# Kernel tuning notes

Measured on AMD Instinct MI355X. Metric: run time of the kernel, lower is better.

The kernel has to match this reference:

```python
import jax, jax.numpy as jnp
import numpy as np

ID_LENGTH = 4   # number of identity images cached in the id bank
HEADS = 20      # SDXL attention heads at channel 1280
SA32 = 0.5


def setup_inputs() -> dict:
    key = jax.random.key(0)
    ks = jax.random.split(key, 7)
    B2, T, C = 8, 576, 1280            # 2*id_length images, 576 tokens each (768/32)^2
    S = ID_LENGTH * T                   # 2304 grouped sequence length
    hidden_states = jax.random.normal(ks[0], (B2, T, C), jnp.float32)
    # cal_attn_mask_xl: one random row pattern repeated, with each image's own
    # block forced True (sliced to the [:id_length*T, :id_length*T] write-mode mask)
    row_pat = jax.random.uniform(ks[1], (1, S)) < SA32
    mask = jnp.tile(row_pat, (S, 1))
    img = jnp.arange(S) // T
    mask = mask | (img[:, None] == img[None, :])
    w = lambda k: jax.random.normal(k, (C, C), jnp.float32) * 0.02
    return {
        "hidden_states": hidden_states,
        "mask": mask,
        "Wq": w(ks[2]), "Wk": w(ks[3]), "Wv": w(ks[4]), "Wo": w(ks[5]),
        "bo": jnp.zeros((C,), jnp.float32),
    }


def reference(hidden_states, mask, Wq, Wk, Wv, Wo, bo):
    # __call1__ path: regroup [2*id_length, T, C] -> [2, id_length*T, C]
    B2, T, C = hidden_states.shape
    hs = hidden_states.reshape(2, ID_LENGTH * T, C)
    hd = C // HEADS

    def split_heads(x):  # [2, S, C] -> [2, H, S, hd]
        return x.reshape(2, -1, HEADS, hd).transpose(0, 2, 1, 3)

    q = split_heads(hs @ Wq)
    k = split_heads(hs @ Wk)   # write mode: encoder_hidden_states == hidden_states
    v = split_heads(hs @ Wv)

    scores = jnp.einsum('bhqd,bhkd->bhqk', q, k) / jnp.sqrt(jnp.asarray(hd, q.dtype))
    scores = jnp.where(mask[None, None], scores, jnp.finfo(scores.dtype).min)
    attnw = jax.nn.softmax(scores, axis=-1)
    out = jnp.einsum('bhqk,bhkd->bhqd', attnw, v)
    out = out.transpose(0, 2, 1, 3).reshape(2, -1, C)
    out = out @ Wo + bo                 # attn.to_out[0]
    return out.reshape(B2, T, C)
```

## Files before the change

kernel.cpp:

```cpp
#include <hip/hip_runtime.h>
#include <hip/hip_bf16.h>
#include <stdint.h>
#include <math.h>

#define S_TOT 2304
#define C_DIM 1280
#define NHEAD 20
#define HD    64
#define M_TOT 4608
#define BH_STRIDE (S_TOT * HD)
#define SC_ROWS 2624
#define KC_STRIDE (SC_ROWS * 64)
#define LOG2E 1.44269504088896f
#define C_SC  (0.125f * LOG2E)
#define MFIX  12.0f

typedef __attribute__((ext_vector_type(8))) short bf16x8;
typedef __attribute__((ext_vector_type(4))) float f32x4;

__device__ __forceinline__ short f2bf(float f) {
    union { float f; uint32_t u; } v; v.f = f;
    uint32_t r = v.u + 0x7FFFu + ((v.u >> 16) & 1u);
    return (short)(r >> 16);
}

__device__ __forceinline__ uint32_t pack2bf(float a, float b) {
    __hip_bfloat162 h = __float22bfloat162_rn(make_float2(a, b));
    union { __hip_bfloat162 h; uint32_t u; } cv; cv.h = h; return cv.u;
}

__device__ __forceinline__ f32x4 zero4() {
    f32x4 z; z[0] = 0.f; z[1] = 0.f; z[2] = 0.f; z[3] = 0.f; return z;
}

__device__ __forceinline__ void gload_lds16(const void* g, void* l) {
    __builtin_amdgcn_global_load_lds(
        (const __attribute__((address_space(1))) uint32_t*)g,
        (__attribute__((address_space(3))) uint32_t*)l, 16, 0, 0);
}

__global__ __launch_bounds__(256)
void prologue(const float* __restrict__ hs, short* __restrict__ hsb,
              const float* __restrict__ W0, const float* __restrict__ W1,
              const float* __restrict__ W2, const float* __restrict__ W3,
              short* __restrict__ T0, short* __restrict__ T1,
              short* __restrict__ T2, short* __restrict__ T3,
              const int* __restrict__ mask, int* __restrict__ hdr,
              int* __restrict__ destmap) {
    __shared__ float tile[32][33];
    __shared__ unsigned long long wbits[36];
    __shared__ int pp[36], dd[36], hb[9];

    const int bx = blockIdx.x;
    const int t = threadIdx.x;

    if (bx < 2880) {
        const int i = bx * 256 + t;
        const float4 v0 = reinterpret_cast<const float4*>(hs)[i * 2];
        const float4 v1 = reinterpret_cast<const float4*>(hs)[i * 2 + 1];
        bf16x8 o;
        o[0] = f2bf(v0.x); o[1] = f2bf(v0.y); o[2] = f2bf(v0.z); o[3] = f2bf(v0.w);
        o[4] = f2bf(v1.x); o[5] = f2bf(v1.y); o[6] = f2bf(v1.z); o[7] = f2bf(v1.w);
        reinterpret_cast<bf16x8*>(hsb)[i] = o;
    } else if (bx < 9280) {
        int id = bx - 2880;
        const int z = id / 1600; id -= z * 1600;
        const int by = id / 40, bxx = id - by * 40;
        const float* W; short* T;
        switch (z) {
            case 0:  W = W0; T = T0; break;
            case 1:  W = W1; T = T1; break;
            case 2:  W = W2; T = T2; break;
            default: W = W3; T = T3; break;
        }
        const int tx = t & 31, ty = t >> 5;
        const int k0 = by * 32, n0 = bxx * 32;
#pragma unroll
        for (int i = 0; i < 4; ++i)
            tile[ty + i * 8][tx] = W[(size_t)(k0 + ty + i * 8) * C_DIM + n0 + tx];
        __syncthreads();
#pragma unroll
        for (int i = 0; i < 4; ++i)
            T[(size_t)(n0 + ty + i * 8) * C_DIM + k0 + tx] = f2bf(tile[tx][ty + i * 8]);
    } else {
        for (int it = 0; it < 9; ++it) {
            const int k = it * 256 + t;
            const int src = (k < 1152) ? 1152 : 0;
            const bool pat = mask[(size_t)src * S_TOT + k] != 0;
            unsigned long long b = __ballot(pat);
            if ((t & 63) == 0) wbits[it * 4 + (t >> 6)] = b;
        }
        __syncthreads();
        if (t == 0) {
            int pcum = 0, dcum[4] = {0, 0, 0, 0};
            for (int wdx = 0; wdx < 36; ++wdx) {
                const int img = wdx / 9;
                const int pc = __popcll(wbits[wdx]);
                pp[wdx] = pcum; dd[wdx] = dcum[img];
                pcum += pc; dcum[img] += 64 - pc;
            }
            hb[0] = pcum;
            int base = (pcum + 63) & ~63;
            for (int i = 0; i < 4; ++i) {
                hb[1 + i] = base; hb[5 + i] = dcum[i];
                base += (dcum[i] + 63) & ~63;
            }
            for (int i = 0; i < 9; ++i) hdr[i] = hb[i];
        }
        __syncthreads();
        if (t < 36) {
            const unsigned long long w64 = wbits[t];
            const int img = t / 9;
            const int pbase = pp[t], dbase = hb[1 + img] + dd[t];
            int pc = 0, dc = 0;
            for (int b = 0; b < 64; ++b) {
                if ((w64 >> b) & 1) destmap[t * 64 + b] = pbase + (pc++);
                else                destmap[t * 64 + b] = dbase + (dc++);
            }
        }
    }
}

__global__ __launch_bounds__(256)
void zero_pads(const int* __restrict__ hdr, short* __restrict__ Kc,
               short* __restrict__ Vr) {
    const int bh = blockIdx.x;
    const int t = threadIdx.x;
    short* Kb = Kc + (size_t)bh * KC_STRIDE;
    short* Vb = Vr + (size_t)bh * KC_STRIDE;
    for (int seg = 0; seg < 5; ++seg) {
        const int cnt = (seg == 0) ? hdr[0] : hdr[4 + seg];
        const int sb  = (seg == 0) ? 0      : hdr[seg];
        const int s0 = sb + cnt;
        const int nrows = ((cnt + 63) & ~63) - cnt;
        for (int idx = t; idx < nrows * 64; idx += 256) {
            const int r = idx >> 6, d = idx & 63;
            Kb[(size_t)(s0 + r) * 64 + d] = 0;
            Vb[(size_t)(s0 + r) * 64 + d] = 0;
        }
    }
}

__global__ __launch_bounds__(256)
void transp_v(const short* __restrict__ Vr, short* __restrict__ Vc) {
    __shared__ short tile[64][72];
    const int bh = blockIdx.y;
    const int s0 = blockIdx.x * 64;
    const int t = threadIdx.x;
    const short* src = Vr + (size_t)bh * KC_STRIDE;
    short* dst = Vc + (size_t)bh * KC_STRIDE;

#pragma unroll
    for (int i = 0; i < 2; ++i) {
        const int e = (i * 256 + t) * 8;
        const int r = e >> 6, c = e & 63;
        bf16x8 v = *(const bf16x8*)(src + (size_t)(s0 + r) * 64 + c);
        *(bf16x8*)&tile[r][c] = v;
    }
    __syncthreads();
    const int d = t & 63, c0 = (t >> 6) * 16;
    short tmp[16];
#pragma unroll
    for (int j = 0; j < 16; ++j) tmp[j] = tile[c0 + j][d];
    *(bf16x8*)(dst + (size_t)d * SC_ROWS + s0 + c0) = *(const bf16x8*)tmp;
    *(bf16x8*)(dst + (size_t)d * SC_ROWS + s0 + c0 + 8) = *(const bf16x8*)(tmp + 8);
}

__device__ __forceinline__ void gemm_core(const short* __restrict__ A,
                                          const short* __restrict__ Wt,
                                          int m0, int n0,
                                          f32x4 acc[4][4],
                                          short* AsB, short* BsB) {
    const int t = threadIdx.x;
    const int lane = t & 63, w = t >> 6;
    const int g = lane >> 4, l15 = lane & 15;
    const int wm = w >> 1, wn = w & 1;

#pragma unroll
    for (int mi = 0; mi < 4; ++mi)
#pragma unroll
        for (int ni = 0; ni < 4; ++ni) acc[mi][ni] = zero4();

    auto stage = [&](int k0, int buf) {
#pragma unroll
        for (int i = 0; i < 4; ++i) {
            const int F = i * 4096 + t * 16;
            const int row = F >> 7;
            const int b = F & 127;
            const int colb = b ^ ((row & 7) << 4);
            gload_lds16((const char*)A + ((size_t)(m0 + row) * C_DIM + k0) * 2 + colb,
                        (char*)AsB + buf * 16384 + F);
            gload_lds16((const char*)Wt + ((size_t)(n0 + row) * C_DIM + k0) * 2 + colb,
                        (char*)BsB + buf * 16384 + F);
        }
    };

    stage(0, 0);
    asm volatile("s_waitcnt vmcnt(0)" ::: "memory");
    __builtin_amdgcn_s_barrier();
    __builtin_amdgcn_sched_barrier(0);

    int cur = 0;
    for (int k0 = 0; k0 < C_DIM; k0 += 64) {
        if (k0 + 64 < C_DIM) stage(k0 + 64, cur ^ 1);
        const char* Ac = (const char*)AsB + cur * 16384;
        const char* Bc = (const char*)BsB + cur * 16384;
#pragma unroll
        for (int ks = 0; ks < 2; ++ks) {
            const int kb = ks * 64 + g * 16;
            bf16x8 af[4], bfr[4];
#pragma unroll
            for (int mi = 0; mi < 4; ++mi) {
                const int row = wm * 64 + mi * 16 + l15;
                af[mi] = *(const bf16x8*)(Ac + row * 128 + (kb ^ ((row & 7) << 4)));
            }
#pragma unroll
            for (int ni = 0; ni < 4; ++ni) {
                const int row = wn * 64 + ni * 16 + l15;
                bfr[ni] = *(const bf16x8*)(Bc + row * 128 + (kb ^ ((row & 7) << 4)));
            }
            __builtin_amdgcn_s_setprio(1);
#pragma unroll
            for (int mi = 0; mi < 4; ++mi)
#pragma unroll
                for (int ni = 0; ni < 4; ++ni)
                    acc[mi][ni] = __builtin_amdgcn_mfma_f32_16x16x32_bf16(
                        af[mi], bfr[ni], acc[mi][ni], 0, 0, 0);
            __builtin_amdgcn_s_setprio(0);
        }
        asm volatile("s_waitcnt vmcnt(0)" ::: "memory");
        __builtin_amdgcn_s_barrier();
        __builtin_amdgcn_sched_barrier(0);
        cur ^= 1;
    }
}

__global__ __launch_bounds__(256)
void gemm_qkv(const short* __restrict__ hsb,
              const short* __restrict__ Wtq, const short* __restrict__ Wtk,
              const short* __restrict__ Wtv, const int* __restrict__ destmap,
              short* __restrict__ Qb, short* __restrict__ Kc, short* __restrict__ Vr) {
    __shared__ short As[2 * 128 * 64];
    __shared__ short Bs[2 * 128 * 64];
    __shared__ int dm[128];
    const int z = blockIdx.z;
    const short* Wt = (z == 0) ? Wtq : (z == 1) ? Wtk : Wtv;
    const int n0 = blockIdx.x * 128, m0 = blockIdx.y * 128;
    const int t = threadIdx.x;

    if (z != 0 && t < 128) {
        const int s0 = (m0 >= S_TOT) ? m0 - S_TOT : m0;
        dm[t] = destmap[s0 + t];
    }

    f32x4 acc[4][4];
    gemm_core(hsb, Wt, m0, n0, acc, As, Bs);

    const int lane = t & 63, w = t >> 6, g = lane >> 4, l15 = lane & 15;
    const int wm = w >> 1, wn = w & 1;
#pragma unroll
    for (int mi = 0; mi < 4; ++mi)
#pragma unroll
        for (int ni = 0; ni < 4; ++ni)
#pragma unroll
            for (int r = 0; r < 4; ++r) {
                const int m = m0 + wm * 64 + mi * 16 + g * 4 + r;
                const int n = n0 + wn * 64 + ni * 16 + l15;
                const int bg = (m >= S_TOT) ? 1 : 0;
                const int s = m - bg * S_TOT;
                const int h = n >> 6, d = n & 63;
                const size_t bh = (size_t)(bg * NHEAD + h);
                float aval = acc[mi][ni][r];
                if (z == 0) aval *= C_SC;
                const short v = f2bf(aval);
                if (z == 0) {
                    Qb[bh * BH_STRIDE + (size_t)s * HD + d] = v;
                } else {
                    const int sc = dm[m - m0];
                    short* dst = (z == 1) ? Kc : Vr;
                    dst[bh * (size_t)KC_STRIDE + (size_t)sc * 64 + d] = v;
                }
            }
}

__global__ __launch_bounds__(256)
void gemm_out(const short* __restrict__ Ab, const short* __restrict__ Wto,
              const float* __restrict__ bo, float* __restrict__ out) {
    __shared__ short As[2 * 128 * 64];
    __shared__ short Bs[2 * 128 * 64];
    const int n0 = blockIdx.x * 128, m0 = blockIdx.y * 128;

    f32x4 acc[4][4];
    gemm_core(Ab, Wto, m0, n0, acc, As, Bs);

    const int t = threadIdx.x;
    const int lane = t & 63, w = t >> 6, g = lane >> 4, l15 = lane & 15;
    const int wm = w >> 1, wn = w & 1;
#pragma unroll
    for (int mi = 0; mi < 4; ++mi)
#pragma unroll
        for (int ni = 0; ni < 4; ++ni) {
            const int n = n0 + wn * 64 + ni * 16 + l15;
            const float bias = bo[n];
#pragma unroll
            for (int r = 0; r < 4; ++r) {
                const int m = m0 + wm * 64 + mi * 16 + g * 4 + r;
                out[(size_t)m * C_DIM + n] = acc[mi][ni][r] + bias;
            }
        }
}

__global__ __launch_bounds__(256)
void attn_mfma(const short* __restrict__ Qb, const short* __restrict__ Kc,
               const short* __restrict__ Vc, const int* __restrict__ hdr,
               short* __restrict__ Ab) {
    __shared__ short Ks[2][4096];
    __shared__ short Vs[2][4096];
    __shared__ short Ps[4096];

    const int t = threadIdx.x;
    const int lane = t & 63, w = t >> 6, g = lane >> 4, l15 = lane & 15;
    const int q0 = blockIdx.x * 64, h = blockIdx.y, b = blockIdx.z;
    const size_t bh = (size_t)(b * NHEAD + h);
    const int qimg = blockIdx.x / 9;

    const int cntp  = hdr[0];
    const int dbase = hdr[1 + qimg];
    const int cntd  = hdr[5 + qimg];
    const int ntp = (cntp + 63) >> 6, ntd = (cntd + 63) >> 6, nt = ntp + ntd;

    const short* Qp = Qb + bh * BH_STRIDE;
    const short* Kp = Kc + bh * (size_t)KC_STRIDE;
    const short* Vp = Vc + bh * (size_t)KC_STRIDE;

    bf16x8 qf[2];
    {
        const int row = q0 + w * 16 + l15;
        qf[0] = *(const bf16x8*)(Qp + (size_t)row * HD + g * 8);
        qf[1] = *(const bf16x8*)(Qp + (size_t)row * HD + 32 + g * 8);
    }

    bf16x8 onesv;
#pragma unroll
    for (int j = 0; j < 8; ++j) onesv[j] = (short)0x3F80;

    const f32x4 sinit = {-MFIX, -MFIX, -MFIX, -MFIX};
    f32x4 o_acc[4], lacc;
#pragma unroll
    for (int df = 0; df < 4; ++df) o_acc[df] = zero4();
    lacc = zero4();

    const int rowP = w * 16 + l15;
    const int swzP = (rowP & 7) << 4;
    const int ckbase = g * 4;

    auto stage = [&](int start, int bufsel) {
#pragma unroll
        for (int i = 0; i < 2; ++i) {
            const int F = i * 4096 + t * 16;
            const int row = F >> 7, bb = F & 127;
            const int colb = bb ^ ((row & 7) << 4);
            gload_lds16((const char*)Kp + (size_t)(start + row) * 128 + colb,
                        (char*)Ks[bufsel] + F);
            gload_lds16((const char*)Vp + (size_t)row * (SC_ROWS * 2) + start * 2 + colb,
                        (char*)Vs[bufsel] + F);
        }
    };

    stage(0, 0);
    asm volatile("s_waitcnt vmcnt(0)" ::: "memory");
    __builtin_amdgcn_s_barrier();
    __builtin_amdgcn_sched_barrier(0);

    int cur = 0;
    for (int tt = 0; tt < nt; ++tt) {
        if (tt + 1 < nt) {
            const int nx = tt + 1;
            const int start = (nx < ntp) ? nx * 64 : dbase + (nx - ntp) * 64;
            stage(start, cur ^ 1);
        }
        const int lim = (tt < ntp) ? cntp - tt * 64 : cntd - (tt - ntp) * 64;

        f32x4 sacc[4];
#pragma unroll
        for (int nf = 0; nf < 4; ++nf) sacc[nf] = sinit;
        __builtin_amdgcn_s_setprio(1);
#pragma unroll
        for (int ks = 0; ks < 2; ++ks) {
            const int kb = ks * 64 + g * 16;
#pragma unroll
            for (int nf = 0; nf < 4; ++nf) {
                const int row = nf * 16 + l15;
                bf16x8 kf = *(const bf16x8*)((const char*)Ks[cur] + row * 128 + (kb ^ ((row & 7) << 4)));
                sacc[nf] = __builtin_amdgcn_mfma_f32_16x16x32_bf16(kf, qf[ks], sacc[nf], 0, 0, 0);
            }
        }
        __builtin_amdgcn_s_setprio(0);

        if (lim < 64) {
#pragma unroll
            for (int nf = 0; nf < 4; ++nf)
#pragma unroll
                for (int r = 0; r < 4; ++r)
                    if (nf * 16 + ckbase + r >= lim) sacc[nf][r] = -1e30f;
        }

#pragma unroll
        for (int nf = 0; nf < 4; ++nf) {
            uint2 u;
            u.x = pack2bf(__builtin_amdgcn_exp2f(sacc[nf][0]),
                          __builtin_amdgcn_exp2f(sacc[nf][1]));
            u.y = pack2bf(__builtin_amdgcn_exp2f(sacc[nf][2]),
                          __builtin_amdgcn_exp2f(sacc[nf][3]));
            *(uint2*)((char*)Ps + rowP * 128 + ((nf * 32 + g * 8) ^ swzP)) = u;
        }

        __builtin_amdgcn_s_setprio(1);
#pragma unroll
        for (int ks = 0; ks < 2; ++ks) {
            const int kb = ks * 64 + g * 16;
            bf16x8 pf = *(const bf16x8*)((const char*)Ps + rowP * 128 + (kb ^ swzP));
            lacc = __builtin_amdgcn_mfma_f32_16x16x32_bf16(onesv, pf, lacc, 0, 0, 0);
#pragma unroll
            for (int df = 0; df < 4; ++df) {
                const int rowV = df * 16 + l15;
                bf16x8 vf = *(const bf16x8*)((const char*)Vs[cur] + rowV * 128 + (kb ^ ((rowV & 7) << 4)));
                o_acc[df] = __builtin_amdgcn_mfma_f32_16x16x32_bf16(vf, pf, o_acc[df], 0, 0, 0);
            }
        }
        __builtin_amdgcn_s_setprio(0);

        asm volatile("s_waitcnt vmcnt(0)" ::: "memory");
        __builtin_amdgcn_s_barrier();
        __builtin_amdgcn_sched_barrier(0);
        cur ^= 1;
    }

    const float inv = 1.f / lacc[0];
    const int rowg = b * S_TOT + q0 + w * 16 + l15;
#pragma unroll
    for (int df = 0; df < 4; ++df) {
        uint2 u;
        u.x = pack2bf(o_acc[df][0] * inv, o_acc[df][1] * inv);
        u.y = pack2bf(o_acc[df][2] * inv, o_acc[df][3] * inv);
        *(uint2*)(Ab + (size_t)rowg * C_DIM + h * 64 + df * 16 + g * 4) = u;
    }
}

extern "C" void kernel_launch(void* const* d_in, const int* in_sizes, int n_in,
                              void* d_out, int out_size, void* d_ws, size_t ws_size,
                              hipStream_t stream)
{
    const float* hs   = (const float*)d_in[0];
    const int*   mask = (const int*)  d_in[1];
    const float* Wq   = (const float*)d_in[2];
    const float* Wk   = (const float*)d_in[3];
    const float* Wv   = (const float*)d_in[4];
    const float* Wo   = (const float*)d_in[5];
    const float* bo   = (const float*)d_in[6];
    float* out = (float*)d_out;

    char* ws = (char*)d_ws;
    const size_t mat_b = (size_t)M_TOT * C_DIM * 2;
    const size_t w_b   = (size_t)C_DIM * C_DIM * 2;
    const size_t kc_b  = (size_t)40 * KC_STRIDE * 2;

    short* hsb = (short*)ws;                 ws += mat_b;
    short* Wtq = (short*)ws;                 ws += w_b;
    short* Wtk = (short*)ws;                 ws += w_b;
    short* Wtv = (short*)ws;                 ws += w_b;
    short* Wto = (short*)ws;                 ws += w_b;
    short* Qb  = (short*)ws;                 ws += mat_b;
    short* Kc  = (short*)ws;                 ws += kc_b;
    short* Vr  = (short*)ws;                 ws += kc_b;
    short* Vc  = (short*)ws;                 ws += kc_b;
    short* Ab  = (short*)ws;                 ws += mat_b;
    int*   hdr = (int*)ws;                   ws += 64;
    int*   destmap = (int*)ws;               ws += S_TOT * 4;

    prologue<<<9281, 256, 0, stream>>>(hs, hsb, Wq, Wk, Wv, Wo,
                                       Wtq, Wtk, Wtv, Wto, mask, hdr, destmap);
    zero_pads<<<40, 256, 0, stream>>>(hdr, Kc, Vr);

    gemm_qkv<<<dim3(C_DIM / 128, M_TOT / 128, 3), 256, 0, stream>>>(
        hsb, Wtq, Wtk, Wtv, destmap, Qb, Kc, Vr);

    transp_v<<<dim3(SC_ROWS / 64, 40), 256, 0, stream>>>(Vr, Vc);

    attn_mfma<<<dim3(S_TOT / 64, NHEAD, 2), 256, 0, stream>>>(Qb, Kc, Vc, hdr, Ab);

    gemm_out<<<dim3(C_DIM / 128, M_TOT / 128), 256, 0, stream>>>(Ab, Wto, bo, out);
}
```

Baseline: 206.2 us.

## Fuse Q/K/V projections into one GEMM kernel sharing the A tile

Replaces the three-way blockIdx.z QKV GEMM with one kernel in which each block loads an activation tile once and multiplies it against the Wq, Wk and Wv tiles together, keeping three accumulator sets. This cuts activation tile loads from global memory by a factor of three and reduces the grid from 1080 to 360 blocks. In exchange the new loop is single-buffered with no load/compute overlap, and tripling the accumulators raises register pressure, which lowers occupancy and parallelism across the GPU.

```diff
diff --git a/kernel.cpp b/kernel.cpp
--- a/kernel.cpp
+++ b/kernel.cpp
@@ -166,6 +166,114 @@
     *(bf16x8*)(dst + (size_t)d * SC_ROWS + s0 + c0 + 8) = *(const bf16x8*)(tmp + 8);
 }
 
+__global__ __launch_bounds__(256, 2)
+void gemm_qkv3(const short* __restrict__ hsb,
+               const short* __restrict__ Wtq, const short* __restrict__ Wtk,
+               const short* __restrict__ Wtv, const int* __restrict__ destmap,
+               short* __restrict__ Qb, short* __restrict__ Kc, short* __restrict__ Vr) {
+    __shared__ short As[128 * 64];
+    __shared__ short Bs[3 * 128 * 64];
+    __shared__ int dm[128];
+
+    const int n0 = blockIdx.x * 128, m0 = blockIdx.y * 128;
+    const int t = threadIdx.x;
+    const int lane = t & 63, w = t >> 6;
+    const int g = lane >> 4, l15 = lane & 15;
+    const int wm = w >> 1, wn = w & 1;
+
+    if (t < 128) {
+        const int s0 = (m0 >= S_TOT) ? m0 - S_TOT : m0;
+        dm[t] = destmap[s0 + t];
+    }
+
+    f32x4 acc[3][4][4];
+#pragma unroll
+    for (int z = 0; z < 3; ++z)
+#pragma unroll
+        for (int mi = 0; mi < 4; ++mi)
+#pragma unroll
+            for (int ni = 0; ni < 4; ++ni) acc[z][mi][ni] = zero4();
+
+    for (int k0 = 0; k0 < C_DIM; k0 += 64) {
+        __syncthreads();
+#pragma unroll
+        for (int i = 0; i < 4; ++i) {
+            const int F = i * 4096 + t * 16;
+            const int row = F >> 7;
+            const int colb = (F & 127) ^ ((row & 7) << 4);
+            gload_lds16((const char*)hsb + ((size_t)(m0 + row) * C_DIM + k0) * 2 + colb,
+                        (char*)As + F);
+        }
+#pragma unroll
+        for (int z = 0; z < 3; ++z) {
+            const short* Wt = (z == 0) ? Wtq : (z == 1) ? Wtk : Wtv;
+#pragma unroll
+            for (int i = 0; i < 4; ++i) {
+                const int F = i * 4096 + t * 16;
+                const int row = F >> 7;
+                const int colb = (F & 127) ^ ((row & 7) << 4);
+                gload_lds16((const char*)Wt + ((size_t)(n0 + row) * C_DIM + k0) * 2 + colb,
+                            (char*)Bs + z * 16384 + F);
+            }
+        }
+        __syncthreads();
+
+#pragma unroll
+        for (int ks = 0; ks < 2; ++ks) {
+            const int kb = ks * 64 + g * 16;
+            bf16x8 af[4];
+#pragma unroll
+            for (int mi = 0; mi < 4; ++mi) {
+                const int row = wm * 64 + mi * 16 + l15;
+                af[mi] = *(const bf16x8*)((const char*)As + row * 128 + (kb ^ ((row & 7) << 4)));
+            }
+#pragma unroll
+            for (int z = 0; z < 3; ++z) {
+                bf16x8 bfr[4];
+#pragma unroll
+                for (int ni = 0; ni < 4; ++ni) {
+                    const int row = wn * 64 + ni * 16 + l15;
+                    bfr[ni] = *(const bf16x8*)((const char*)Bs + z * 16384 + row * 128 + (kb ^ ((row & 7) << 4)));
+                }
+                __builtin_amdgcn_s_setprio(1);
+#pragma unroll
+                for (int mi = 0; mi < 4; ++mi)
+#pragma unroll
+                    for (int ni = 0; ni < 4; ++ni)
+                        acc[z][mi][ni] = __builtin_amdgcn_mfma_f32_16x16x32_bf16(
+                            af[mi], bfr[ni], acc[z][mi][ni], 0, 0, 0);
+                __builtin_amdgcn_s_setprio(0);
+            }
+        }
+    }
+
+#pragma unroll
+    for (int z = 0; z < 3; ++z)
+#pragma unroll
+        for (int mi = 0; mi < 4; ++mi)
+#pragma unroll
+            for (int ni = 0; ni < 4; ++ni)
+#pragma unroll
+                for (int r = 0; r < 4; ++r) {
+                    const int m = m0 + wm * 64 + mi * 16 + g * 4 + r;
+                    const int n = n0 + wn * 64 + ni * 16 + l15;
+                    const int bg = (m >= S_TOT) ? 1 : 0;
+                    const int s = m - bg * S_TOT;
+                    const int h = n >> 6, d = n & 63;
+                    const size_t bh = (size_t)(bg * NHEAD + h);
+                    float aval = acc[z][mi][ni][r];
+                    if (z == 0) aval *= C_SC;
+                    const short v = f2bf(aval);
+                    if (z == 0) {
+                        Qb[bh * BH_STRIDE + (size_t)s * HD + d] = v;
+                    } else {
+                        const int sc = dm[m - m0];
+                        short* dst = (z == 1) ? Kc : Vr;
+                        dst[bh * (size_t)KC_STRIDE + (size_t)sc * 64 + d] = v;
+                    }
+                }
+}
+
 __device__ __forceinline__ void gemm_core(const short* __restrict__ A,
                                           const short* __restrict__ Wt,
                                           int m0, int n0,
@@ -233,54 +341,6 @@
         __builtin_amdgcn_sched_barrier(0);
         cur ^= 1;
     }
-}
-
-__global__ __launch_bounds__(256)
-void gemm_qkv(const short* __restrict__ hsb,
-              const short* __restrict__ Wtq, const short* __restrict__ Wtk,
-              const short* __restrict__ Wtv, const int* __restrict__ destmap,
-              short* __restrict__ Qb, short* __restrict__ Kc, short* __restrict__ Vr) {
-    __shared__ short As[2 * 128 * 64];
-    __shared__ short Bs[2 * 128 * 64];
-    __shared__ int dm[128];
-    const int z = blockIdx.z;
-    const short* Wt = (z == 0) ? Wtq : (z == 1) ? Wtk : Wtv;
-    const int n0 = blockIdx.x * 128, m0 = blockIdx.y * 128;
-    const int t = threadIdx.x;
-
-    if (z != 0 && t < 128) {
-        const int s0 = (m0 >= S_TOT) ? m0 - S_TOT : m0;
-        dm[t] = destmap[s0 + t];
-    }
-
-    f32x4 acc[4][4];
-    gemm_core(hsb, Wt, m0, n0, acc, As, Bs);
-
-    const int lane = t & 63, w = t >> 6, g = lane >> 4, l15 = lane & 15;
-    const int wm = w >> 1, wn = w & 1;
-#pragma unroll
-    for (int mi = 0; mi < 4; ++mi)
-#pragma unroll
-        for (int ni = 0; ni < 4; ++ni)
-#pragma unroll
-            for (int r = 0; r < 4; ++r) {
-                const int m = m0 + wm * 64 + mi * 16 + g * 4 + r;
-                const int n = n0 + wn * 64 + ni * 16 + l15;
-                const int bg = (m >= S_TOT) ? 1 : 0;
-                const int s = m - bg * S_TOT;
-                const int h = n >> 6, d = n & 63;
-                const size_t bh = (size_t)(bg * NHEAD + h);
-                float aval = acc[mi][ni][r];
-                if (z == 0) aval *= C_SC;
-                const short v = f2bf(aval);
-                if (z == 0) {
-                    Qb[bh * BH_STRIDE + (size_t)s * HD + d] = v;
-                } else {
-                    const int sc = dm[m - m0];
-                    short* dst = (z == 1) ? Kc : Vr;
-                    dst[bh * (size_t)KC_STRIDE + (size_t)sc * 64 + d] = v;
-                }
-            }
 }
 
 __global__ __launch_bounds__(256)
@@ -482,7 +542,7 @@
                                        Wtq, Wtk, Wtv, Wto, mask, hdr, destmap);
     zero_pads<<<40, 256, 0, stream>>>(hdr, Kc, Vr);
 
-    gemm_qkv<<<dim3(C_DIM / 128, M_TOT / 128, 3), 256, 0, stream>>>(
+    gemm_qkv3<<<dim3(C_DIM / 128, M_TOT / 128), 256, 0, stream>>>(
         hsb, Wtq, Wtk, Wtv, destmap, Qb, Kc, Vr);
 
     transp_v<<<dim3(SC_ROWS / 64, 40), 256, 0, stream>>>(Vr, Vc);
```

After: 187.7 us. -8.9%, faster.
